# Performance work log

Hardware: AMD Instinct MI355X
Metric: run time of the kernel (lower is better)

The kernel has to match this reference:

```python
import jax, jax.numpy as jnp
import numpy as np

N = 100000     # total points
PBS = 500      # point_batch_size (hard-coded in module)
K = 100        # num_neighbors
KP = 15        # num_kernel_points
EPS = 1e-5


def _bn(x, g, b, axes):
    # torch BatchNorm in training mode: batch stats, biased variance
    m = jnp.mean(x, axis=axes, keepdims=True)
    v = jnp.var(x, axis=axes, keepdims=True)
    return (x - m) / jnp.sqrt(v + EPS) * g + b


def setup_inputs() -> dict:
    key = jax.random.key(0)
    ks = jax.random.split(key, 16)
    rn = lambda k, sh, s=1.0: jax.random.normal(k, sh, jnp.float32) * s
    return {
        "pts": rn(ks[0], (N, 3)),
        "normal": rn(ks[1], (N, 3)),
        "kp_points": rn(ks[2], (KP, 3)),
        "kp_weights": rn(ks[3], (KP, 3, 128), 0.3),
        "kp_sigma": jnp.float32(1.0),
        "conv1_w": rn(ks[4], (1024, 128), 128 ** -0.5),
        "conv1_b": rn(ks[5], (1024,), 0.02),
        "bn1_g": jnp.ones((1024,), jnp.float32),
        "bn1_b": jnp.zeros((1024,), jnp.float32),
        "fc1_w": rn(ks[6], (512, 1024), 1024 ** -0.5),
        "fc1_b": rn(ks[7], (512,), 0.02),
        "bn4_g": jnp.ones((512,), jnp.float32),
        "bn4_b": jnp.zeros((512,), jnp.float32),
        "fc2_w": rn(ks[8], (256, 512), 512 ** -0.5),
        "fc2_b": rn(ks[9], (256,), 0.02),
        "bn5_g": jnp.ones((256,), jnp.float32),
        "bn5_b": jnp.zeros((256,), jnp.float32),
        "fc3_w": rn(ks[10], (3, 256), 256 ** -0.5),
        "fc3_b": rn(ks[11], (3,), 0.02),
        "index": jax.random.randint(ks[12], (PBS,), 0, N, jnp.int32),
    }


def reference(pts, normal, kp_points, kp_weights, kp_sigma,
              conv1_w, conv1_b, bn1_g, bn1_b,
              fc1_w, fc1_b, bn4_g, bn4_b,
              fc2_w, fc2_b, bn5_g, bn5_b,
              fc3_w, fc3_b, index):
    sel = pts[index]                                               # [B,3]
    # L-inf pairwise distance and kNN (topk of -dist, as in the torch code)
    dist = jnp.max(jnp.abs(sel[:, None, :] - pts[None, :, :]), axis=-1)  # [B,N]
    _, nbr = jax.lax.top_k(-dist, K)                               # [B,K]
    rel = pts[nbr] - sel[:, None, :]                               # [B,K,3]

    # KPConv: gaussian weights vs kernel points, per-kernel-point linear map
    d2 = jnp.sum((rel[:, :, None, :] - kp_points[None, None]) ** 2, axis=-1)  # [B,K,KP]
    w = jnp.exp(-0.5 * d2 / (kp_sigma ** 2))
    wf = rel[:, :, None, :] * w[..., None]                         # [B,K,KP,3]
    h = jax.nn.relu(jnp.einsum('bnkc,kco->bno', wf, kp_weights))   # [B,K,128]

    # 1x1 conv 128->1024, relu then BN over (batch, points) per channel
    h = jnp.einsum('bnc,oc->bno', h, conv1_w) + conv1_b            # [B,K,1024]
    h = _bn(jax.nn.relu(h), bn1_g, bn1_b, (0, 1))
    feat = jnp.max(h, axis=1)                                      # [B,1024]

    feat = _bn(jax.nn.relu(feat @ fc1_w.T + fc1_b), bn4_g, bn4_b, (0,))
    feat = _bn(jax.nn.relu(feat @ fc2_w.T + fc2_b), bn5_g, bn5_b, (0,))
    feat = feat @ fc3_w.T + fc3_b                                  # [B,3]
    return feat, normal[index]
```

## Files before the change

### kernel.cpp

```cpp
#include <hip/hip_runtime.h>
#include <hip/hip_fp16.h>

#define NPTS 100000
#define NB 500
#define KNN 100
#define KPN 15
#define C1 128
#define C2 1024
#define C3 512
#define C4 256

#define G 64
#define NCELLS (G * G * G)
#define GB 5.0f
#define GINVH ((float)G / (2.f * GB))
#define CAND_CAP 2048

typedef _Float16 half8 __attribute__((ext_vector_type(8)));
typedef float f32x4 __attribute__((ext_vector_type(4)));

__device__ __forceinline__ int cell_coord(float x) {
  int c = (int)floorf((x + GB) * GINVH);
  return min(max(c, 0), G - 1);
}
__device__ __forceinline__ int cell_of(float x, float y, float z) {
  return (cell_coord(x) << 12) | (cell_coord(y) << 6) | cell_coord(z);
}

__global__ __launch_bounds__(256) void prep_kernel(
    const float* __restrict__ pts, const float* __restrict__ normal,
    const int* __restrict__ index, const float* __restrict__ w1,
    const float* __restrict__ kpw, const float* __restrict__ fc1w,
    const float* __restrict__ fc2w, float* __restrict__ sel,
    float* __restrict__ out2, __half* __restrict__ wh,
    __half* __restrict__ kpwT_hi, __half* __restrict__ kpwT_lo,
    __half* __restrict__ fwhi, __half* __restrict__ fwlo,
    __half* __restrict__ f2whi, __half* __restrict__ f2wlo,
    unsigned* __restrict__ cnt) {
  int i = blockIdx.x * 256 + threadIdx.x;
  if (i < NB) {
    int ix = index[i];
    sel[i * 3 + 0] = pts[3 * ix + 0];
    sel[i * 3 + 1] = pts[3 * ix + 1];
    sel[i * 3 + 2] = pts[3 * ix + 2];
    out2[i * 3 + 0] = normal[3 * ix + 0];
    out2[i * 3 + 1] = normal[3 * ix + 1];
    out2[i * 3 + 2] = normal[3 * ix + 2];
  }
  if (i < C2 * C1 / 4) {
    float4 v = *(const float4*)&w1[i * 4];
    __half hb[4] = {__float2half(v.x), __float2half(v.y), __float2half(v.z),
                    __float2half(v.w)};
    *(float2*)&wh[i * 4] = *(float2*)hb;
  }
  if (i < 128 * 64 / 4) {
#pragma unroll
    for (int k = 0; k < 4; ++k) {
      int e = i * 4 + k;
      int o = e >> 6, j = e & 63;
      float v = (j < 45) ? kpw[j * 128 + o] : 0.f;
      __half hi = __float2half_rn(v);
      kpwT_hi[e] = hi;
      kpwT_lo[e] = __float2half_rn(v - __half2float(hi));
    }
  }
  if (i < C3 * C2 / 4) {
    float4 v = *(const float4*)&fc1w[i * 4];
    float vv[4] = {v.x, v.y, v.z, v.w};
    __half hb[4], lb[4];
#pragma unroll
    for (int k = 0; k < 4; ++k) {
      __half hi = __float2half_rn(vv[k]);
      hb[k] = hi;
      lb[k] = __float2half_rn(vv[k] - __half2float(hi));
    }
    *(float2*)&fwhi[i * 4] = *(float2*)hb;
    *(float2*)&fwlo[i * 4] = *(float2*)lb;
  }
  if (i < C4 * C3 / 4) {
    float4 v = *(const float4*)&fc2w[i * 4];
    float vv[4] = {v.x, v.y, v.z, v.w};
    __half hb[4], lb[4];
#pragma unroll
    for (int k = 0; k < 4; ++k) {
      __half hi = __float2half_rn(vv[k]);
      hb[k] = hi;
      lb[k] = __float2half_rn(vv[k] - __half2float(hi));
    }
    *(float2*)&f2whi[i * 4] = *(float2*)hb;
    *(float2*)&f2wlo[i * 4] = *(float2*)lb;
  }
  if (i < NPTS / 4) {
    float4 a = *(const float4*)&pts[i * 12];
    float4 b = *(const float4*)&pts[i * 12 + 4];
    float4 c = *(const float4*)&pts[i * 12 + 8];
    atomicAdd(&cnt[cell_of(a.x, a.y, a.z)], 1u);
    atomicAdd(&cnt[cell_of(a.w, b.x, b.y)], 1u);
    atomicAdd(&cnt[cell_of(b.z, b.w, c.x)], 1u);
    atomicAdd(&cnt[cell_of(c.y, c.z, c.w)], 1u);
  }
}

__global__ __launch_bounds__(256) void grid_scan_kernel(
    const unsigned* __restrict__ cnt, unsigned* __restrict__ cursor,
    unsigned* __restrict__ gbase) {
  const int tid = threadIdx.x;
  int base = blockIdx.x * 1024 + tid * 4;
  unsigned c0 = cnt[base], c1 = cnt[base + 1], c2 = cnt[base + 2],
           c3 = cnt[base + 3];
  unsigned tot = c0 + c1 + c2 + c3;
  __shared__ unsigned sb[256];
  __shared__ unsigned s_base;
  sb[tid] = tot;
  __syncthreads();
  for (int off = 1; off < 256; off <<= 1) {
    unsigned add = (tid >= off) ? sb[tid - off] : 0u;
    __syncthreads();
    sb[tid] += add;
    __syncthreads();
  }
  if (tid == 255) s_base = atomicAdd(gbase, sb[255]);
  __syncthreads();
  unsigned excl = s_base + sb[tid] - tot;
  cursor[base] = excl;
  cursor[base + 1] = excl + c0;
  cursor[base + 2] = excl + c0 + c1;
  cursor[base + 3] = excl + c0 + c1 + c2;
}

__global__ __launch_bounds__(256) void grid_scatter_kernel(
    const float* __restrict__ pts, unsigned* __restrict__ cursor,
    float4* __restrict__ sorted) {
  int i = blockIdx.x * 256 + threadIdx.x;
  if (i >= NPTS) return;
  float x = pts[3 * i], y = pts[3 * i + 1], z = pts[3 * i + 2];
  unsigned pos = atomicAdd(&cursor[cell_of(x, y, z)], 1u);
  sorted[pos] = make_float4(x, y, z, __int_as_float(i));
}

__device__ __forceinline__ unsigned linf_bits(float px, float py, float pz,
                                              float sx, float sy, float sz) {
  float dx = fabsf(px - sx), dy = fabsf(py - sy), dz = fabsf(pz - sz);
  return __float_as_uint(fmaxf(fmaxf(dx, dy), dz));
}

__global__ __launch_bounds__(256) void knn_kernel(
    const float4* __restrict__ sorted, const unsigned* __restrict__ cnt,
    const unsigned* __restrict__ cursor,
    const float* __restrict__ sel, int* __restrict__ nbr) {
  const int b = blockIdx.x;
  const int tid = threadIdx.x;
  __shared__ unsigned cbits[CAND_CAP];
  __shared__ int cidx[CAND_CAP];
  __shared__ unsigned hist[4096];
  __shared__ unsigned scanbuf[256];
  __shared__ int s_total, s_m, s_mc, s_chunk;
  __shared__ unsigned s_excl, s_bub;

  const float qx = sel[b * 3 + 0], qy = sel[b * 3 + 1], qz = sel[b * 3 + 2];
  const int qcx = cell_coord(qx), qcy = cell_coord(qy), qcz = cell_coord(qz);

  if (tid == 0) s_total = 0;
  __syncthreads();
  int s = 1;
  int pxlo = 1, pxhi = 0, pylo = 1, pyhi = 0, pzlo = 1, pzhi = 0;
  int xlo, xhi, ylo, yhi, zlo, zhi;
  for (;;) {
    xlo = max(qcx - s, 0); xhi = min(qcx + s, G - 1);
    ylo = max(qcy - s, 0); yhi = min(qcy + s, G - 1);
    zlo = max(qcz - s, 0); zhi = min(qcz + s, G - 1);
    int nx = xhi - xlo + 1, ny = yhi - ylo + 1, nz = zhi - zlo + 1;
    int ncell = nx * ny * nz;
    unsigned local = 0;
    for (int ci = tid; ci < ncell; ci += 256) {
      int cz = ci % nz;
      int r = ci / nz;
      int cy = r % ny;
      int cx = r / ny;
      int ax = xlo + cx, ay = ylo + cy, az = zlo + cz;
      if (ax >= pxlo && ax <= pxhi && ay >= pylo && ay <= pyhi &&
          az >= pzlo && az <= pzhi)
        continue;
      local += cnt[(ax << 12) | (ay << 6) | az];
    }
#pragma unroll
    for (int off = 32; off; off >>= 1) local += __shfl_down(local, off);
    if ((tid & 63) == 0) atomicAdd(&s_total, (int)local);
    __syncthreads();
    if (s_total >= KNN || (xlo == 0 && ylo == 0 && zlo == 0 && xhi == G - 1 &&
                           yhi == G - 1 && zhi == G - 1))
      break;
    pxlo = xlo; pxhi = xhi; pylo = ylo; pyhi = yhi; pzlo = zlo; pzhi = zhi;
    ++s;
    __syncthreads();
  }

  if (tid == 0) s_m = 0;
  __syncthreads();
  {
    int nx = xhi - xlo + 1, ny = yhi - ylo + 1, nz = zhi - zlo + 1;
    int ncell = nx * ny * nz;
    for (int ci = tid; ci < ncell; ci += 256) {
      int cz = ci % nz;
      int r = ci / nz;
      int cy = r % ny;
      int cx = r / ny;
      int cell = ((xlo + cx) << 12) | ((ylo + cy) << 6) | (zlo + cz);
      unsigned end = cursor[cell];
      unsigned beg = end - cnt[cell];
      int k = (int)(end - beg);
      if (k > 0) {
        int e0 = atomicAdd(&s_m, k);
        for (unsigned p = beg; p < end; ++p, ++e0) {
          if (e0 < CAND_CAP) {
            float4 f = sorted[p];
            cbits[e0] = linf_bits(f.x, f.y, f.z, qx, qy, qz);
            cidx[e0] = __float_as_int(f.w);
          }
        }
      }
    }
  }
  __syncthreads();
  int m = s_m < CAND_CAP ? s_m : CAND_CAP;

  for (int j = tid; j < 4096; j += 256) hist[j] = 0;
  __syncthreads();
  for (int e = tid; e < m; e += 256) atomicAdd(&hist[cbits[e] >> 19], 1u);
  __syncthreads();
  unsigned csum = 0;
  {
    int c0 = tid * 16;
#pragma unroll
    for (int j = 0; j < 16; ++j) csum += hist[c0 + j];
  }
  scanbuf[tid] = csum;
  __syncthreads();
  for (int off = 1; off < 256; off <<= 1) {
    unsigned add = (tid >= off) ? scanbuf[tid - off] : 0u;
    __syncthreads();
    scanbuf[tid] += add;
    __syncthreads();
  }
  {
    unsigned incl = scanbuf[tid], excl = incl - csum;
    if (excl < KNN && KNN <= incl) {
      s_chunk = tid;
      s_excl = excl;
    }
  }
  __syncthreads();
  if (tid == 0) {
    unsigned cum = s_excl;
    int bin = s_chunk * 16;
    while (cum + hist[bin] < KNN) {
      cum += hist[bin];
      ++bin;
    }
    s_bub = (unsigned)(bin + 1) << 19;
  }
  __syncthreads();

  const unsigned bub = s_bub;
  const float dub = __uint_as_float(bub);
  int xlo2 = min(max((int)floorf((qx - dub + GB) * GINVH), 0), G - 1);
  int xhi2 = min(max((int)floorf((qx + dub + GB) * GINVH), 0), G - 1);
  int ylo2 = min(max((int)floorf((qy - dub + GB) * GINVH), 0), G - 1);
  int yhi2 = min(max((int)floorf((qy + dub + GB) * GINVH), 0), G - 1);
  int zlo2 = min(max((int)floorf((qz - dub + GB) * GINVH), 0), G - 1);
  int zhi2 = min(max((int)floorf((qz + dub + GB) * GINVH), 0), G - 1);
  const bool nested = (s_m <= CAND_CAP) && xlo2 >= xlo && xhi2 <= xhi &&
                      ylo2 >= ylo && yhi2 <= yhi && zlo2 >= zlo && zhi2 <= zhi;

  int mc;
  if (nested) {
    if (tid == 0) s_mc = 0;
    __syncthreads();
    unsigned kb[8];
    int ki[8];
    int nloc = 0;
    for (int c = tid; c < m; c += 256) {
      unsigned bc = cbits[c];
      if (bc < bub) {
        kb[nloc] = bc;
        ki[nloc] = cidx[c];
        ++nloc;
      }
    }
    int base = 0;
    if (nloc) base = atomicAdd(&s_mc, nloc);
    __syncthreads();
    for (int j = 0; j < nloc; ++j) {
      cbits[base + j] = kb[j];
      cidx[base + j] = ki[j];
    }
    __syncthreads();
    mc = s_mc;
  } else {
    if (tid == 0) s_mc = 0;
    __syncthreads();
    {
      int nx = xhi2 - xlo2 + 1, ny = yhi2 - ylo2 + 1, nz = zhi2 - zlo2 + 1;
      int ncell = nx * ny * nz;
      for (int ci = tid; ci < ncell; ci += 256) {
        int cz = ci % nz;
        int r = ci / nz;
        int cy = r % ny;
        int cx = r / ny;
        int cell = ((xlo2 + cx) << 12) | ((ylo2 + cy) << 6) | (zlo2 + cz);
        unsigned end = cursor[cell];
        unsigned beg = end - cnt[cell];
        for (unsigned p = beg; p < end; ++p) {
          float4 f = sorted[p];
          unsigned bits = linf_bits(f.x, f.y, f.z, qx, qy, qz);
          if (bits < bub) {
            int e = atomicAdd(&s_mc, 1);
            if (e < CAND_CAP) {
              cbits[e] = bits;
              cidx[e] = __float_as_int(f.w);
            }
          }
        }
      }
    }
    __syncthreads();
    mc = s_mc < CAND_CAP ? s_mc : CAND_CAP;
  }

  for (int c = tid; c < mc; c += 256) {
    unsigned bc = cbits[c];
    int ic = cidx[c];
    int rank = 0;
    for (int j = 0; j < mc; ++j) {
      unsigned bj = cbits[j];
      rank += (bj < bc || (bj == bc && cidx[j] < ic)) ? 1 : 0;
    }
    if (rank < KNN) nbr[b * KNN + rank] = ic;
  }
}

__global__ __launch_bounds__(512, 2) void kpconv_conv1_kernel(
    const float* __restrict__ pts, const float* __restrict__ sel,
    const int* __restrict__ nbr, const float* __restrict__ kp_points,
    const __half* __restrict__ kpwT_hi, const __half* __restrict__ kpwT_lo,
    const float* __restrict__ kp_sigma, const __half* __restrict__ wh,
    const float* __restrict__ bias, float* __restrict__ featmax,
    float* __restrict__ featmin, float* __restrict__ featsum,
    float* __restrict__ featsq) {
  const int b = blockIdx.x;
  const int tid = threadIdx.x;
  const int wave = tid >> 6, lane = tid & 63;
  const int lr = lane & 15, quad = lane >> 4;

  __shared__ __align__(16) char smem[71168];
  __half* As_hi = (__half*)smem;
  __half* As_lo = As_hi + 112 * 72;
  __half* Bs_hi = As_lo + 112 * 72;
  __half* Bs_lo = Bs_hi + 128 * 72;
  float* rel = (float*)(Bs_lo + 128 * 72);
  float* kpp = rel + 100 * 4;
  __half* Hs = (__half*)smem;

  for (int i = tid; i < 128 * 8; i += 512) {
    int row = i >> 3, seg = i & 7;
    *(float4*)&Bs_hi[row * 72 + seg * 8] =
        *(const float4*)&kpwT_hi[row * 64 + seg * 8];
    *(float4*)&Bs_lo[row * 72 + seg * 8] =
        *(const float4*)&kpwT_lo[row * 64 + seg * 8];
  }
  {
    float4 z = make_float4(0.f, 0.f, 0.f, 0.f);
    for (int i = tid; i < 112 * 8; i += 512) {
      int row = i >> 3, seg = i & 7;
      *(float4*)&As_hi[row * 72 + seg * 8] = z;
      *(float4*)&As_lo[row * 72 + seg * 8] = z;
    }
  }
  if (tid < 45) kpp[tid] = kp_points[tid];
  if (tid < 100) {
    int idx = nbr[b * KNN + tid];
    rel[tid * 4 + 0] = pts[3 * idx + 0] - sel[b * 3 + 0];
    rel[tid * 4 + 1] = pts[3 * idx + 1] - sel[b * 3 + 1];
    rel[tid * 4 + 2] = pts[3 * idx + 2] - sel[b * 3 + 2];
  }
  __syncthreads();

  const float sg = kp_sigma[0];
  const float inv2s2 = -0.5f / (sg * sg);
  for (int i = tid; i < 100 * KPN; i += 512) {
    int k = i / KPN, p = i - k * KPN;
    float rx = rel[k * 4 + 0] - kpp[p * 3 + 0];
    float ry = rel[k * 4 + 1] - kpp[p * 3 + 1];
    float rz = rel[k * 4 + 2] - kpp[p * 3 + 2];
    float w = expf(inv2s2 * (rx * rx + ry * ry + rz * rz));
#pragma unroll
    for (int c = 0; c < 3; ++c) {
      float a = rel[k * 4 + c] * w;
      __half hi = __float2half_rn(a);
      As_hi[k * 72 + p * 3 + c] = hi;
      As_lo[k * 72 + p * 3 + c] = __float2half_rn(a - __half2float(hi));
    }
  }
  __syncthreads();

  f32x4 acc1[7];
#pragma unroll
  for (int m = 0; m < 7; ++m) acc1[m] = (f32x4)(0.f);
#pragma unroll
  for (int s = 0; s < 2; ++s) {
    int boff = (wave * 16 + lr) * 72 + s * 32 + quad * 8;
    half8 bhi = *(const half8*)&Bs_hi[boff];
    half8 blo = *(const half8*)&Bs_lo[boff];
#pragma unroll
    for (int m = 0; m < 7; ++m) {
      int aoff = (m * 16 + lr) * 72 + s * 32 + quad * 8;
      half8 ahi = *(const half8*)&As_hi[aoff];
      half8 alo = *(const half8*)&As_lo[aoff];
      acc1[m] = __builtin_amdgcn_mfma_f32_16x16x32_f16(ahi, bhi, acc1[m], 0, 0, 0);
      acc1[m] = __builtin_amdgcn_mfma_f32_16x16x32_f16(ahi, blo, acc1[m], 0, 0, 0);
      acc1[m] = __builtin_amdgcn_mfma_f32_16x16x32_f16(alo, bhi, acc1[m], 0, 0, 0);
    }
  }
  __syncthreads();

  {
    int col = wave * 16 + lr;
#pragma unroll
    for (int m = 0; m < 7; ++m)
#pragma unroll
      for (int r = 0; r < 4; ++r) {
        int row = m * 16 + quad * 4 + r;
        Hs[row * 136 + col] = __float2half_rn(fmaxf(acc1[m][r], 0.f));
      }
  }
  __syncthreads();

  half8 afr[4][7];
#pragma unroll
  for (int s = 0; s < 4; ++s)
#pragma unroll
    for (int m = 0; m < 7; ++m)
      afr[s][m] = *(const half8*)&Hs[(m * 16 + lr) * 136 + s * 32 + quad * 8];

  const int wrow = wave * 16 + lr;
  half8 bcur[4];
#pragma unroll
  for (int s = 0; s < 4; ++s)
    bcur[s] = *(const half8*)&wh[wrow * 128 + s * 32 + quad * 8];

  for (int c = 0; c < 8; ++c) {
    half8 bnxt[4];
    if (c + 1 < 8) {
#pragma unroll
      for (int s = 0; s < 4; ++s)
        bnxt[s] = *(const half8*)&wh[((c + 1) * 128 + wrow) * 128 + s * 32 +
                                     quad * 8];
    }

    f32x4 acc2[7];
#pragma unroll
    for (int m = 0; m < 7; ++m) acc2[m] = (f32x4)(0.f);
#pragma unroll
    for (int s = 0; s < 4; ++s)
#pragma unroll
      for (int m = 0; m < 7; ++m)
        acc2[m] = __builtin_amdgcn_mfma_f32_16x16x32_f16(afr[s][m], bcur[s],
                                                         acc2[m], 0, 0, 0);

    {
      int col = c * 128 + wrow;
      float bv = bias[col];
      float pmax = -1e30f, pmin = 1e30f, psum = 0.f, psq = 0.f;
#pragma unroll
      for (int m = 0; m < 7; ++m)
#pragma unroll
        for (int r = 0; r < 4; ++r) {
          int row = m * 16 + quad * 4 + r;
          if (row < 100) {
            float y = fmaxf(acc2[m][r] + bv, 0.f);
            pmax = fmaxf(pmax, y);
            pmin = fminf(pmin, y);
            psum += y;
            psq += y * y;
          }
        }
      pmax = fmaxf(pmax, __shfl_xor(pmax, 16));
      pmax = fmaxf(pmax, __shfl_xor(pmax, 32));
      pmin = fminf(pmin, __shfl_xor(pmin, 16));
      pmin = fminf(pmin, __shfl_xor(pmin, 32));
      psum += __shfl_xor(psum, 16);
      psum += __shfl_xor(psum, 32);
      psq += __shfl_xor(psq, 16);
      psq += __shfl_xor(psq, 32);
      if (quad == 0) {
        featmax[b * C2 + col] = pmax;
        featmin[b * C2 + col] = pmin;
        featsum[b * C2 + col] = psum;
        featsq[b * C2 + col] = psq;
      }
    }
#pragma unroll
    for (int s = 0; s < 4; ++s) bcur[s] = bnxt[s];
  }
}

__global__ __launch_bounds__(256) void stats1_kernel(
    const float* __restrict__ featsum, const float* __restrict__ featsq,
    float* __restrict__ bnsum, float* __restrict__ bnsq) {
  int col = blockIdx.x * 256 + threadIdx.x;
  int r0 = blockIdx.y * 50;
  float s = 0.f, q = 0.f;
  for (int r = r0; r < r0 + 50; ++r) {
    s += featsum[r * C2 + col];
    q += featsq[r * C2 + col];
  }
  atomicAdd(&bnsum[col], s);
  atomicAdd(&bnsq[col], q);
}

__global__ __launch_bounds__(256) void bn1half_kernel(
    const float* __restrict__ featmax, const float* __restrict__ featmin,
    const float* __restrict__ bnsum, const float* __restrict__ bnsq,
    const float* __restrict__ g, const float* __restrict__ bb,
    __half* __restrict__ Xhi, __half* __restrict__ Xlo) {
  int idx = blockIdx.x * 256 + threadIdx.x;
  if (idx >= NB * C2) return;
  int o = idx & (C2 - 1);
  const float invn = 1.f / (float)(NB * KNN);
  float m = bnsum[o] * invn;
  float v = bnsq[o] * invn - m * m;
  float a = g[o] / sqrtf(v + 1e-5f);
  float x = (a >= 0.f) ? featmax[idx] : featmin[idx];
  float y = (x - m) * a + bb[o];
  __half hi = __float2half_rn(y);
  Xhi[idx] = hi;
  Xlo[idx] = __float2half_rn(y - __half2float(hi));
}

__global__ __launch_bounds__(256) void fc1_mfma_kernel(
    const __half* __restrict__ Xhi, const __half* __restrict__ Xlo,
    const __half* __restrict__ Whi, const __half* __restrict__ Wlo,
    const float* __restrict__ bias, float* __restrict__ yraw,
    float* __restrict__ s, float* __restrict__ sq) {
  const int r0 = blockIdx.x * 64;
  const int n0 = blockIdx.y * 64;
  const int tid = threadIdx.x;
  const int wave = tid >> 6, lane = tid & 63;
  const int lr = lane & 15, quad = lane >> 4;
  __shared__ __half Xs_hi[64 * 72], Xs_lo[64 * 72];
  __shared__ __half Ws_hi[64 * 72], Ws_lo[64 * 72];

  f32x4 acc[4];
#pragma unroll
  for (int m = 0; m < 4; ++m) acc[m] = (f32x4)(0.f);

  for (int kc = 0; kc < C2; kc += 64) {
    __syncthreads();
    for (int i = tid; i < 64 * 8; i += 256) {
      int row = i >> 3, seg = i & 7;
      int gr = r0 + row;
      float4 vhi = make_float4(0.f, 0.f, 0.f, 0.f), vlo = vhi;
      if (gr < NB) {
        vhi = *(const float4*)&Xhi[gr * C2 + kc + seg * 8];
        vlo = *(const float4*)&Xlo[gr * C2 + kc + seg * 8];
      }
      *(float4*)&Xs_hi[row * 72 + seg * 8] = vhi;
      *(float4*)&Xs_lo[row * 72 + seg * 8] = vlo;
      *(float4*)&Ws_hi[row * 72 + seg * 8] =
          *(const float4*)&Whi[(n0 + row) * C2 + kc + seg * 8];
      *(float4*)&Ws_lo[row * 72 + seg * 8] =
          *(const float4*)&Wlo[(n0 + row) * C2 + kc + seg * 8];
    }
    __syncthreads();

#pragma unroll
    for (int s2 = 0; s2 < 2; ++s2) {
      int boff = (wave * 16 + lr) * 72 + s2 * 32 + quad * 8;
      half8 bhi = *(const half8*)&Ws_hi[boff];
      half8 blo = *(const half8*)&Ws_lo[boff];
#pragma unroll
      for (int m = 0; m < 4; ++m) {
        int aoff = (m * 16 + lr) * 72 + s2 * 32 + quad * 8;
        half8 ahi = *(const half8*)&Xs_hi[aoff];
        half8 alo = *(const half8*)&Xs_lo[aoff];
        acc[m] = __builtin_amdgcn_mfma_f32_16x16x32_f16(ahi, bhi, acc[m], 0, 0, 0);
        acc[m] = __builtin_amdgcn_mfma_f32_16x16x32_f16(ahi, blo, acc[m], 0, 0, 0);
        acc[m] = __builtin_amdgcn_mfma_f32_16x16x32_f16(alo, bhi, acc[m], 0, 0, 0);
      }
    }
  }

  {
    int col = n0 + wave * 16 + lr;
    float bv = bias[col];
    float psum = 0.f, psq = 0.f;
#pragma unroll
    for (int m = 0; m < 4; ++m)
#pragma unroll
      for (int r = 0; r < 4; ++r) {
        int row = r0 + m * 16 + quad * 4 + r;
        if (row < NB) {
          float y = fmaxf(acc[m][r] + bv, 0.f);
          yraw[row * C3 + col] = y;
          psum += y;
          psq += y * y;
        }
      }
    psum += __shfl_xor(psum, 16);
    psum += __shfl_xor(psum, 32);
    psq += __shfl_xor(psq, 16);
    psq += __shfl_xor(psq, 32);
    if (quad == 0) {
      atomicAdd(&s[col], psum);
      atomicAdd(&sq[col], psq);
    }
  }
}

__global__ __launch_bounds__(256) void fc2_mfma_kernel(
    const float* __restrict__ x,
    const float* __restrict__ bnsum4, const float* __restrict__ bnsq4,
    const float* __restrict__ g, const float* __restrict__ bb,
    const __half* __restrict__ Whi, const __half* __restrict__ Wlo,
    const float* __restrict__ bias, float* __restrict__ yraw,
    float* __restrict__ s, float* __restrict__ sq) {
  const int r0 = blockIdx.x * 64;
  const int n0 = blockIdx.y * 64;
  const int tid = threadIdx.x;
  const int wave = tid >> 6, lane = tid & 63;
  const int lr = lane & 15, quad = lane >> 4;
  __shared__ __half Xs_hi[64 * 72], Xs_lo[64 * 72];
  __shared__ __half Ws_hi[64 * 72], Ws_lo[64 * 72];
  __shared__ float amul[C3], badd[C3];

  {
    const float invn = 1.f / (float)NB;
    for (int o = tid; o < C3; o += 256) {
      float m = bnsum4[o] * invn;
      float v = bnsq4[o] * invn - m * m;
      float a = g[o] / sqrtf(v + 1e-5f);
      amul[o] = a;
      badd[o] = bb[o] - m * a;
    }
  }

  f32x4 acc[4];
#pragma unroll
  for (int m = 0; m < 4; ++m) acc[m] = (f32x4)(0.f);

  for (int kc = 0; kc < C3; kc += 64) {
    __syncthreads();
    for (int i = tid; i < 64 * 8; i += 256) {
      int row = i >> 3, seg = i & 7;
      int gr = r0 + row;
      __half hbuf[8], lbuf[8];
      if (gr < NB) {
        float4 a0 = *(const float4*)&x[gr * C3 + kc + seg * 8];
        float4 a1 = *(const float4*)&x[gr * C3 + kc + seg * 8 + 4];
        float vals[8] = {a0.x, a0.y, a0.z, a0.w, a1.x, a1.y, a1.z, a1.w};
#pragma unroll
        for (int j = 0; j < 8; ++j) {
          int o = kc + seg * 8 + j;
          float y = vals[j] * amul[o] + badd[o];
          __half hi = __float2half_rn(y);
          hbuf[j] = hi;
          lbuf[j] = __float2half_rn(y - __half2float(hi));
        }
      } else {
#pragma unroll
        for (int j = 0; j < 8; ++j) {
          hbuf[j] = __float2half_rn(0.f);
          lbuf[j] = __float2half_rn(0.f);
        }
      }
      *(float4*)&Xs_hi[row * 72 + seg * 8] = *(float4*)hbuf;
      *(float4*)&Xs_lo[row * 72 + seg * 8] = *(float4*)lbuf;
      *(float4*)&Ws_hi[row * 72 + seg * 8] =
          *(const float4*)&Whi[(n0 + row) * C3 + kc + seg * 8];
      *(float4*)&Ws_lo[row * 72 + seg * 8] =
          *(const float4*)&Wlo[(n0 + row) * C3 + kc + seg * 8];
    }
    __syncthreads();

#pragma unroll
    for (int s2 = 0; s2 < 2; ++s2) {
      int boff = (wave * 16 + lr) * 72 + s2 * 32 + quad * 8;
      half8 bhi = *(const half8*)&Ws_hi[boff];
      half8 blo = *(const half8*)&Ws_lo[boff];
#pragma unroll
      for (int m = 0; m < 4; ++m) {
        int aoff = (m * 16 + lr) * 72 + s2 * 32 + quad * 8;
        half8 ahi = *(const half8*)&Xs_hi[aoff];
        half8 alo = *(const half8*)&Xs_lo[aoff];
        acc[m] = __builtin_amdgcn_mfma_f32_16x16x32_f16(ahi, bhi, acc[m], 0, 0, 0);
        acc[m] = __builtin_amdgcn_mfma_f32_16x16x32_f16(ahi, blo, acc[m], 0, 0, 0);
        acc[m] = __builtin_amdgcn_mfma_f32_16x16x32_f16(alo, bhi, acc[m], 0, 0, 0);
      }
    }
  }

  {
    int col = n0 + wave * 16 + lr;
    float bv = bias[col];
    float psum = 0.f, psq = 0.f;
#pragma unroll
    for (int m = 0; m < 4; ++m)
#pragma unroll
      for (int r = 0; r < 4; ++r) {
        int row = r0 + m * 16 + quad * 4 + r;
        if (row < NB) {
          float y = fmaxf(acc[m][r] + bv, 0.f);
          yraw[row * C4 + col] = y;
          psum += y;
          psq += y * y;
        }
      }
    psum += __shfl_xor(psum, 16);
    psum += __shfl_xor(psum, 32);
    psq += __shfl_xor(psq, 16);
    psq += __shfl_xor(psq, 32);
    if (quad == 0) {
      atomicAdd(&s[col], psum);
      atomicAdd(&sq[col], psq);
    }
  }
}

__global__ __launch_bounds__(256) void fc3_kernel(
    const float* __restrict__ x,
    const float* __restrict__ bnsum, const float* __restrict__ bnsq,
    const float* __restrict__ g, const float* __restrict__ bb,
    const float* __restrict__ w, const float* __restrict__ bias,
    float* __restrict__ out) {
  const int tid = threadIdx.x;
  __shared__ float pmul[C4], padd[C4];
  {
    const float invn = 1.f / (float)NB;
    float m = bnsum[tid] * invn;
    float v = bnsq[tid] * invn - m * m;
    float a = g[tid] / sqrtf(v + 1e-5f);
    pmul[tid] = a;
    padd[tid] = bb[tid] - m * a;
  }
  __syncthreads();
  int idx = blockIdx.x * 256 + tid;
  if (idx >= NB * 3) return;
  int b = idx / 3, o = idx % 3;
  float acc = 0.f;
  for (int k = 0; k < C4; ++k)
    acc += (x[b * C4 + k] * pmul[k] + padd[k]) * w[o * C4 + k];
  out[idx] = acc + bias[o];
}

extern "C" void kernel_launch(void* const* d_in, const int* in_sizes, int n_in,
                              void* d_out, int out_size, void* d_ws,
                              size_t ws_size, hipStream_t stream) {
  const float* pts = (const float*)d_in[0];
  const float* normal = (const float*)d_in[1];
  const float* kp_points = (const float*)d_in[2];
  const float* kp_weights = (const float*)d_in[3];
  const float* kp_sigma = (const float*)d_in[4];
  const float* conv1_w = (const float*)d_in[5];
  const float* conv1_b = (const float*)d_in[6];
  const float* bn1_g = (const float*)d_in[7];
  const float* bn1_b = (const float*)d_in[8];
  const float* fc1_w = (const float*)d_in[9];
  const float* fc1_b = (const float*)d_in[10];
  const float* bn4_g = (const float*)d_in[11];
  const float* bn4_b = (const float*)d_in[12];
  const float* fc2_w = (const float*)d_in[13];
  const float* fc2_b = (const float*)d_in[14];
  const float* bn5_g = (const float*)d_in[15];
  const float* bn5_b = (const float*)d_in[16];
  const float* fc3_w = (const float*)d_in[17];
  const float* fc3_b = (const float*)d_in[18];
  const int* index = (const int*)d_in[19];
  float* out = (float*)d_out;

  char* p = (char*)d_ws;
  auto carve = [&](size_t bytes) {
    void* r = (void*)p;
    p += (bytes + 255) & ~(size_t)255;
    return r;
  };
  float* sel = (float*)carve(NB * 3 * 4);
  int* nbr = (int*)carve(NB * KNN * 4);
  __half* wh = (__half*)carve((size_t)C2 * C1 * 2);
  __half* kpwT_hi = (__half*)carve((size_t)128 * 64 * 2);
  __half* kpwT_lo = (__half*)carve((size_t)128 * 64 * 2);
  __half* fwhi = (__half*)carve((size_t)C3 * C2 * 2);
  __half* fwlo = (__half*)carve((size_t)C3 * C2 * 2);
  __half* f2whi = (__half*)carve((size_t)C4 * C3 * 2);
  __half* f2wlo = (__half*)carve((size_t)C4 * C3 * 2);
  __half* Xhi = (__half*)carve((size_t)NB * C2 * 2);
  __half* Xlo = (__half*)carve((size_t)NB * C2 * 2);
  float* featmax = (float*)carve(NB * C2 * 4);
  float* featmin = (float*)carve(NB * C2 * 4);
  float* featsum = (float*)carve(NB * C2 * 4);
  float* featsq = (float*)carve(NB * C2 * 4);
  float* f2raw = (float*)carve(NB * C3 * 4);
  float* f3raw = (float*)carve(NB * C4 * 4);
  float* stats = (float*)carve((2 * C2 + 2 * C3 + 2 * C4 + 64) * 4);
  float* bnsum = stats;
  float* bnsq = stats + C2;
  float* s4 = stats + 2 * C2;
  float* sq4 = s4 + C3;
  float* s5 = sq4 + C3;
  float* sq5 = s5 + C4;
  unsigned* gbase = (unsigned*)(stats + 2 * C2 + 2 * C3 + 2 * C4);
  unsigned* cellcnt = (unsigned*)carve((size_t)NCELLS * 4);
  unsigned* cellcur = (unsigned*)carve((size_t)NCELLS * 4);
  float4* sortedpts = (float4*)carve((size_t)NPTS * 16);

  hipMemsetAsync(stats, 0, (2 * C2 + 2 * C3 + 2 * C4 + 64) * 4, stream);
  hipMemsetAsync(cellcnt, 0, (size_t)NCELLS * 4, stream);

  prep_kernel<<<(C3 * C2 / 4 + 255) / 256, 256, 0, stream>>>(
      pts, normal, index, conv1_w, kp_weights, fc1_w, fc2_w, sel,
      out + NB * 3, wh, kpwT_hi, kpwT_lo, fwhi, fwlo, f2whi, f2wlo, cellcnt);
  grid_scan_kernel<<<256, 256, 0, stream>>>(cellcnt, cellcur, gbase);
  grid_scatter_kernel<<<(NPTS + 255) / 256, 256, 0, stream>>>(pts, cellcur,
                                                              sortedpts);
  knn_kernel<<<NB, 256, 0, stream>>>(sortedpts, cellcnt, cellcur, sel, nbr);
  kpconv_conv1_kernel<<<NB, 512, 0, stream>>>(
      pts, sel, nbr, kp_points, kpwT_hi, kpwT_lo, kp_sigma, wh, conv1_b,
      featmax, featmin, featsum, featsq);
  stats1_kernel<<<dim3(4, 10), 256, 0, stream>>>(featsum, featsq, bnsum,
                                                 bnsq);
  bn1half_kernel<<<(NB * C2 + 255) / 256, 256, 0, stream>>>(
      featmax, featmin, bnsum, bnsq, bn1_g, bn1_b, Xhi, Xlo);
  fc1_mfma_kernel<<<dim3(8, 8), 256, 0, stream>>>(Xhi, Xlo, fwhi, fwlo, fc1_b,
                                                  f2raw, s4, sq4);
  fc2_mfma_kernel<<<dim3(8, 4), 256, 0, stream>>>(
      f2raw, s4, sq4, bn4_g, bn4_b, f2whi, f2wlo, fc2_b, f3raw, s5, sq5);
  fc3_kernel<<<(NB * 3 + 255) / 256, 256, 0, stream>>>(
      f3raw, s5, sq5, bn5_g, bn5_b, fc3_w, fc3_b, out);
}
```

Baseline: 262.8 us.

## Fuse kNN selection into KPConv/conv1 kernel with shared-memory neighbor handoff

Merges the kNN kernel into the kpconv_conv1 kernel, so one 512-thread block per query does the grid search, selection and the feature MLP, handing neighbor indices through shared memory. This removes a kernel launch and the global round trip of the neighbor array, and the kNN phase gains more threads per query. The kNN scratch buffers reuse the same shared memory as the GEMM tiles. In exchange, the kNN phase now runs at the larger kernel's occupancy (launch bounds 512,2 with about 70KB of shared memory). The per-thread compaction buffer also shrinks to 4 entries.

```diff
diff --git a/kernel.cpp b/kernel.cpp
--- a/kernel.cpp
+++ b/kernel.cpp
@@ -144,16 +144,33 @@
   return __float_as_uint(fmaxf(fmaxf(dx, dy), dz));
 }
 
-__global__ __launch_bounds__(256) void knn_kernel(
+__global__ __launch_bounds__(512, 2) void knn_kpconv_conv1_kernel(
     const float4* __restrict__ sorted, const unsigned* __restrict__ cnt,
     const unsigned* __restrict__ cursor,
-    const float* __restrict__ sel, int* __restrict__ nbr) {
+    const float* __restrict__ pts, const float* __restrict__ sel,
+    const float* __restrict__ kp_points, const __half* __restrict__ kpwT_hi,
+    const __half* __restrict__ kpwT_lo, const float* __restrict__ kp_sigma,
+    const __half* __restrict__ wh, const float* __restrict__ bias,
+    float* __restrict__ featmax, float* __restrict__ featmin,
+    float* __restrict__ featsum, float* __restrict__ featsq) {
   const int b = blockIdx.x;
   const int tid = threadIdx.x;
-  __shared__ unsigned cbits[CAND_CAP];
-  __shared__ int cidx[CAND_CAP];
-  __shared__ unsigned hist[4096];
-  __shared__ unsigned scanbuf[256];
+  const int wave = tid >> 6, lane = tid & 63;
+  const int lr = lane & 15, quad = lane >> 4;
+
+  __shared__ __align__(16) char smem[71168];
+  unsigned* cbits = (unsigned*)smem;
+  int* cidx = (int*)(smem + 8192);
+  unsigned* hist = (unsigned*)(smem + 16384);
+  unsigned* scanbuf = (unsigned*)(smem + 32768);
+  __half* As_hi = (__half*)smem;
+  __half* As_lo = As_hi + 112 * 72;
+  __half* Bs_hi = As_lo + 112 * 72;
+  __half* Bs_lo = Bs_hi + 128 * 72;
+  float* rel = (float*)(Bs_lo + 128 * 72);
+  float* kpp = rel + 100 * 4;
+  __half* Hs = (__half*)smem;
+  __shared__ int nbr_s[KNN];
   __shared__ int s_total, s_m, s_mc, s_chunk;
   __shared__ unsigned s_excl, s_bub;
 
@@ -172,7 +189,7 @@
     int nx = xhi - xlo + 1, ny = yhi - ylo + 1, nz = zhi - zlo + 1;
     int ncell = nx * ny * nz;
     unsigned local = 0;
-    for (int ci = tid; ci < ncell; ci += 256) {
+    for (int ci = tid; ci < ncell; ci += 512) {
       int cz = ci % nz;
       int r = ci / nz;
       int cy = r % ny;
@@ -200,7 +217,7 @@
   {
     int nx = xhi - xlo + 1, ny = yhi - ylo + 1, nz = zhi - zlo + 1;
     int ncell = nx * ny * nz;
-    for (int ci = tid; ci < ncell; ci += 256) {
+    for (int ci = tid; ci < ncell; ci += 512) {
       int cz = ci % nz;
       int r = ci / nz;
       int cy = r % ny;
@@ -224,29 +241,31 @@
   __syncthreads();
   int m = s_m < CAND_CAP ? s_m : CAND_CAP;
 
-  for (int j = tid; j < 4096; j += 256) hist[j] = 0;
-  __syncthreads();
-  for (int e = tid; e < m; e += 256) atomicAdd(&hist[cbits[e] >> 19], 1u);
-  __syncthreads();
-  unsigned csum = 0;
+  for (int j = tid; j < 4096; j += 512) hist[j] = 0;
+  __syncthreads();
+  for (int e = tid; e < m; e += 512) atomicAdd(&hist[cbits[e] >> 19], 1u);
+  __syncthreads();
   {
-    int c0 = tid * 16;
-#pragma unroll
-    for (int j = 0; j < 16; ++j) csum += hist[c0 + j];
-  }
-  scanbuf[tid] = csum;
-  __syncthreads();
-  for (int off = 1; off < 256; off <<= 1) {
-    unsigned add = (tid >= off) ? scanbuf[tid - off] : 0u;
-    __syncthreads();
-    scanbuf[tid] += add;
-    __syncthreads();
-  }
-  {
-    unsigned incl = scanbuf[tid], excl = incl - csum;
-    if (excl < KNN && KNN <= incl) {
-      s_chunk = tid;
-      s_excl = excl;
+    unsigned csum = 0;
+    if (tid < 256) {
+      int c0 = tid * 16;
+#pragma unroll
+      for (int j = 0; j < 16; ++j) csum += hist[c0 + j];
+      scanbuf[tid] = csum;
+    }
+    __syncthreads();
+    for (int off = 1; off < 256; off <<= 1) {
+      unsigned add = (tid < 256 && tid >= off) ? scanbuf[tid - off] : 0u;
+      __syncthreads();
+      if (tid < 256) scanbuf[tid] += add;
+      __syncthreads();
+    }
+    if (tid < 256) {
+      unsigned incl = scanbuf[tid], excl = incl - csum;
+      if (excl < KNN && KNN <= incl) {
+        s_chunk = tid;
+        s_excl = excl;
+      }
     }
   }
   __syncthreads();
@@ -276,10 +295,10 @@
   if (nested) {
     if (tid == 0) s_mc = 0;
     __syncthreads();
-    unsigned kb[8];
-    int ki[8];
+    unsigned kb[4];
+    int ki[4];
     int nloc = 0;
-    for (int c = tid; c < m; c += 256) {
+    for (int c = tid; c < m; c += 512) {
       unsigned bc = cbits[c];
       if (bc < bub) {
         kb[nloc] = bc;
@@ -302,7 +321,7 @@
     {
       int nx = xhi2 - xlo2 + 1, ny = yhi2 - ylo2 + 1, nz = zhi2 - zlo2 + 1;
       int ncell = nx * ny * nz;
-      for (int ci = tid; ci < ncell; ci += 256) {
+      for (int ci = tid; ci < ncell; ci += 512) {
         int cz = ci % nz;
         int r = ci / nz;
         int cy = r % ny;
@@ -327,7 +346,7 @@
     mc = s_mc < CAND_CAP ? s_mc : CAND_CAP;
   }
 
-  for (int c = tid; c < mc; c += 256) {
+  for (int c = tid; c < mc; c += 512) {
     unsigned bc = cbits[c];
     int ic = cidx[c];
     int rank = 0;
@@ -335,31 +354,9 @@
       unsigned bj = cbits[j];
       rank += (bj < bc || (bj == bc && cidx[j] < ic)) ? 1 : 0;
     }
-    if (rank < KNN) nbr[b * KNN + rank] = ic;
-  }
-}
-
-__global__ __launch_bounds__(512, 2) void kpconv_conv1_kernel(
-    const float* __restrict__ pts, const float* __restrict__ sel,
-    const int* __restrict__ nbr, const float* __restrict__ kp_points,
-    const __half* __restrict__ kpwT_hi, const __half* __restrict__ kpwT_lo,
-    const float* __restrict__ kp_sigma, const __half* __restrict__ wh,
-    const float* __restrict__ bias, float* __restrict__ featmax,
-    float* __restrict__ featmin, float* __restrict__ featsum,
-    float* __restrict__ featsq) {
-  const int b = blockIdx.x;
-  const int tid = threadIdx.x;
-  const int wave = tid >> 6, lane = tid & 63;
-  const int lr = lane & 15, quad = lane >> 4;
-
-  __shared__ __align__(16) char smem[71168];
-  __half* As_hi = (__half*)smem;
-  __half* As_lo = As_hi + 112 * 72;
-  __half* Bs_hi = As_lo + 112 * 72;
-  __half* Bs_lo = Bs_hi + 128 * 72;
-  float* rel = (float*)(Bs_lo + 128 * 72);
-  float* kpp = rel + 100 * 4;
-  __half* Hs = (__half*)smem;
+    if (rank < KNN) nbr_s[rank] = ic;
+  }
+  __syncthreads();
 
   for (int i = tid; i < 128 * 8; i += 512) {
     int row = i >> 3, seg = i & 7;
@@ -378,10 +375,10 @@
   }
   if (tid < 45) kpp[tid] = kp_points[tid];
   if (tid < 100) {
-    int idx = nbr[b * KNN + tid];
-    rel[tid * 4 + 0] = pts[3 * idx + 0] - sel[b * 3 + 0];
-    rel[tid * 4 + 1] = pts[3 * idx + 1] - sel[b * 3 + 1];
-    rel[tid * 4 + 2] = pts[3 * idx + 2] - sel[b * 3 + 2];
+    int idx = nbr_s[tid];
+    rel[tid * 4 + 0] = pts[3 * idx + 0] - qx;
+    rel[tid * 4 + 1] = pts[3 * idx + 1] - qy;
+    rel[tid * 4 + 2] = pts[3 * idx + 2] - qz;
   }
   __syncthreads();
 
@@ -405,20 +402,20 @@
 
   f32x4 acc1[7];
 #pragma unroll
-  for (int m = 0; m < 7; ++m) acc1[m] = (f32x4)(0.f);
-#pragma unroll
-  for (int s = 0; s < 2; ++s) {
-    int boff = (wave * 16 + lr) * 72 + s * 32 + quad * 8;
+  for (int m2 = 0; m2 < 7; ++m2) acc1[m2] = (f32x4)(0.f);
+#pragma unroll
+  for (int s2 = 0; s2 < 2; ++s2) {
+    int boff = (wave * 16 + lr) * 72 + s2 * 32 + quad * 8;
     half8 bhi = *(const half8*)&Bs_hi[boff];
     half8 blo = *(const half8*)&Bs_lo[boff];
 #pragma unroll
-    for (int m = 0; m < 7; ++m) {
-      int aoff = (m * 16 + lr) * 72 + s * 32 + quad * 8;
+    for (int m2 = 0; m2 < 7; ++m2) {
+      int aoff = (m2 * 16 + lr) * 72 + s2 * 32 + quad * 8;
       half8 ahi = *(const half8*)&As_hi[aoff];
       half8 alo = *(const half8*)&As_lo[aoff];
-      acc1[m] = __builtin_amdgcn_mfma_f32_16x16x32_f16(ahi, bhi, acc1[m], 0, 0, 0);
-      acc1[m] = __builtin_amdgcn_mfma_f32_16x16x32_f16(ahi, blo, acc1[m], 0, 0, 0);
-      acc1[m] = __builtin_amdgcn_mfma_f32_16x16x32_f16(alo, bhi, acc1[m], 0, 0, 0);
+      acc1[m2] = __builtin_amdgcn_mfma_f32_16x16x32_f16(ahi, bhi, acc1[m2], 0, 0, 0);
+      acc1[m2] = __builtin_amdgcn_mfma_f32_16x16x32_f16(ahi, blo, acc1[m2], 0, 0, 0);
+      acc1[m2] = __builtin_amdgcn_mfma_f32_16x16x32_f16(alo, bhi, acc1[m2], 0, 0, 0);
     }
   }
   __syncthreads();
@@ -426,58 +423,60 @@
   {
     int col = wave * 16 + lr;
 #pragma unroll
-    for (int m = 0; m < 7; ++m)
+    for (int m2 = 0; m2 < 7; ++m2)
 #pragma unroll
       for (int r = 0; r < 4; ++r) {
-        int row = m * 16 + quad * 4 + r;
-        Hs[row * 136 + col] = __float2half_rn(fmaxf(acc1[m][r], 0.f));
+        int row = m2 * 16 + quad * 4 + r;
+        Hs[row * 136 + col] = __float2half_rn(fmaxf(acc1[m2][r], 0.f));
       }
   }
   __syncthreads();
 
   half8 afr[4][7];
 #pragma unroll
-  for (int s = 0; s < 4; ++s)
-#pragma unroll
-    for (int m = 0; m < 7; ++m)
-      afr[s][m] = *(const half8*)&Hs[(m * 16 + lr) * 136 + s * 32 + quad * 8];
+  for (int s2 = 0; s2 < 4; ++s2)
+#pragma unroll
+    for (int m2 = 0; m2 < 7; ++m2)
+      afr[s2][m2] =
+          *(const half8*)&Hs[(m2 * 16 + lr) * 136 + s2 * 32 + quad * 8];
 
   const int wrow = wave * 16 + lr;
   half8 bcur[4];
 #pragma unroll
-  for (int s = 0; s < 4; ++s)
-    bcur[s] = *(const half8*)&wh[wrow * 128 + s * 32 + quad * 8];
+  for (int s2 = 0; s2 < 4; ++s2)
+    bcur[s2] = *(const half8*)&wh[wrow * 128 + s2 * 32 + quad * 8];
 
   for (int c = 0; c < 8; ++c) {
     half8 bnxt[4];
     if (c + 1 < 8) {
 #pragma unroll
-      for (int s = 0; s < 4; ++s)
-        bnxt[s] = *(const half8*)&wh[((c + 1) * 128 + wrow) * 128 + s * 32 +
-                                     quad * 8];
+      for (int s2 = 0; s2 < 4; ++s2)
+        bnxt[s2] = *(const half8*)&wh[((c + 1) * 128 + wrow) * 128 + s2 * 32 +
+                                      quad * 8];
     }
 
     f32x4 acc2[7];
 #pragma unroll
-    for (int m = 0; m < 7; ++m) acc2[m] = (f32x4)(0.f);
-#pragma unroll
-    for (int s = 0; s < 4; ++s)
-#pragma unroll
-      for (int m = 0; m < 7; ++m)
-        acc2[m] = __builtin_amdgcn_mfma_f32_16x16x32_f16(afr[s][m], bcur[s],
-                                                         acc2[m], 0, 0, 0);
+    for (int m2 = 0; m2 < 7; ++m2) acc2[m2] = (f32x4)(0.f);
+#pragma unroll
+    for (int s2 = 0; s2 < 4; ++s2)
+#pragma unroll
+      for (int m2 = 0; m2 < 7; ++m2)
+        acc2[m2] = __builtin_amdgcn_mfma_f32_16x16x32_f16(afr[s2][m2],
+                                                          bcur[s2], acc2[m2],
+                                                          0, 0, 0);
 
     {
       int col = c * 128 + wrow;
       float bv = bias[col];
       float pmax = -1e30f, pmin = 1e30f, psum = 0.f, psq = 0.f;
 #pragma unroll
-      for (int m = 0; m < 7; ++m)
+      for (int m2 = 0; m2 < 7; ++m2)
 #pragma unroll
         for (int r = 0; r < 4; ++r) {
-          int row = m * 16 + quad * 4 + r;
+          int row = m2 * 16 + quad * 4 + r;
           if (row < 100) {
-            float y = fmaxf(acc2[m][r] + bv, 0.f);
+            float y = fmaxf(acc2[m2][r] + bv, 0.f);
             pmax = fmaxf(pmax, y);
             pmin = fminf(pmin, y);
             psum += y;
@@ -500,7 +499,7 @@
       }
     }
 #pragma unroll
-    for (int s = 0; s < 4; ++s) bcur[s] = bnxt[s];
+    for (int s2 = 0; s2 < 4; ++s2) bcur[s2] = bnxt[s2];
   }
 }
 
@@ -784,7 +783,6 @@
     return r;
   };
   float* sel = (float*)carve(NB * 3 * 4);
-  int* nbr = (int*)carve(NB * KNN * 4);
   __half* wh = (__half*)carve((size_t)C2 * C1 * 2);
   __half* kpwT_hi = (__half*)carve((size_t)128 * 64 * 2);
   __half* kpwT_lo = (__half*)carve((size_t)128 * 64 * 2);
@@ -821,10 +819,9 @@
   grid_scan_kernel<<<256, 256, 0, stream>>>(cellcnt, cellcur, gbase);
   grid_scatter_kernel<<<(NPTS + 255) / 256, 256, 0, stream>>>(pts, cellcur,
                                                               sortedpts);
-  knn_kernel<<<NB, 256, 0, stream>>>(sortedpts, cellcnt, cellcur, sel, nbr);
-  kpconv_conv1_kernel<<<NB, 512, 0, stream>>>(
-      pts, sel, nbr, kp_points, kpwT_hi, kpwT_lo, kp_sigma, wh, conv1_b,
-      featmax, featmin, featsum, featsq);
+  knn_kpconv_conv1_kernel<<<NB, 512, 0, stream>>>(
+      sortedpts, cellcnt, cellcur, pts, sel, kp_points, kpwT_hi, kpwT_lo,
+      kp_sigma, wh, conv1_b, featmax, featmin, featsum, featsq);
   stats1_kernel<<<dim3(4, 10), 256, 0, stream>>>(featsum, featsq, bnsum,
                                                  bnsq);
   bn1half_kernel<<<(NB * C2 + 255) / 256, 256, 0, stream>>>(
```

New measurement: 277.7 us. +5.7%, slower.
